# Kernel tuning notes

Measured on AMD Instinct MI355X. Metric: run time of the kernel, lower is better.

## Reference

```python
import jax, jax.numpy as jnp
import numpy as np

DIM = 1024
H = 16
D = DIM // H  # head_dim = 64
SCALE = 1.0 / np.sqrt(D)


def setup_inputs() -> dict:
    key = jax.random.key(0)
    ks = jax.random.split(key, 4)
    B, S = 4, 4096
    std = 1.0 / np.sqrt(DIM)
    return {
        "x": jax.random.normal(ks[0], (B, S, DIM), jnp.float32),
        "Wqkv": jax.random.normal(ks[1], (DIM, 3 * DIM), jnp.float32) * std,
        "bqkv": jnp.zeros((3 * DIM,), jnp.float32),
        "Wq": jax.random.normal(ks[2], (DIM, DIM), jnp.float32) * std,
        "bq": jnp.zeros((DIM,), jnp.float32),
        "Wproj": jax.random.normal(ks[3], (DIM, DIM), jnp.float32) * std,
        "bproj": jnp.zeros((DIM,), jnp.float32),
        "num_anchor_tokens": 512,
    }


def reference(x, Wqkv, bqkv, Wq, bq, Wproj, bproj, num_anchor_tokens):
    B, S, _ = x.shape
    A = num_anchor_tokens  # static Python int
    anchors = x[:, :A, :]          # (B, A, DIM)
    queries = x[:, A:, :]          # (B, Q, DIM)
    Q = S - A

    # Anchor tokens: full qkv projection
    qkv = anchors @ Wqkv + bqkv                      # (B, A, 3*DIM)
    qkv = qkv.reshape(B, A, 3, H, D)
    aq = jnp.transpose(qkv[:, :, 0], (0, 2, 1, 3))   # (B, H, A, D)
    ak = jnp.transpose(qkv[:, :, 1], (0, 2, 1, 3))   # (B, H, A, D)
    av = jnp.transpose(qkv[:, :, 2], (0, 2, 1, 3))   # (B, H, A, D)

    # Query tokens: query-only projection
    qq = (queries @ Wq + bq).reshape(B, Q, H, D)
    qq = jnp.transpose(qq, (0, 2, 1, 3))             # (B, H, Q, D)

    q_all = jnp.concatenate([aq, qq], axis=2)        # (B, H, S, D)

    # Everyone attends only to anchor keys/values
    scores = jnp.einsum("bhsd,bhad->bhsa", q_all, ak) * SCALE  # (B, H, S, A)
    attn = jax.nn.softmax(scores, axis=-1)
    out = jnp.einsum("bhsa,bhad->bhsd", attn, av)    # (B, H, S, D)
    out = jnp.transpose(out, (0, 2, 1, 3)).reshape(B, S, DIM)
    return out @ Wproj + bproj
```

## Files before the change

### kernel.cpp

```cpp
#include <hip/hip_runtime.h>
#include <hip/hip_bf16.h>

#define DIMC 1024
#define HC   16
#define DC   64
#define BC   4
#define SC   4096
#define ANC  512
#define QNC  3584
#define GK   1024
#define QSCALE (0.125f * 1.44269504088896f)

typedef __attribute__((ext_vector_type(4))) float f32x4;
typedef __attribute__((ext_vector_type(8))) short s16x8;
typedef __attribute__((ext_vector_type(4))) short s16x4;

__device__ inline short f2bf(float f) {
    unsigned u = __builtin_bit_cast(unsigned, f);
    u += 0x7fff + ((u >> 16) & 1);
    return (short)(u >> 16);
}
__device__ inline unsigned cvtpk(float lo, float hi) {
    unsigned d;
    asm("v_cvt_pk_bf16_f32 %0, %1, %2" : "=v"(d) : "v"(lo), "v"(hi));
    return d;
}

#define GLOAD16(gp, lp) __builtin_amdgcn_global_load_lds( \
    (const __attribute__((address_space(1))) void*)(gp),  \
    (__attribute__((address_space(3))) void*)(lp), 16, 0, 0)

__device__ __forceinline__ void tc_tile(
    const float* __restrict__ W, short* __restrict__ Wt, int K, int N,
    int bx, int by, float (*t)[33])
{
    const int tx = threadIdx.x & 31, ty = threadIdx.x >> 5;
    const int nt = bx * 32, kt = by * 32;
    #pragma unroll
    for (int j = 0; j < 4; ++j)
        t[ty + 8 * j][tx] = W[(size_t)(kt + ty + 8 * j) * N + nt + tx];
    __syncthreads();
    #pragma unroll
    for (int j = 0; j < 4; ++j)
        Wt[(size_t)(nt + ty + 8 * j) * K + kt + tx] = f2bf(t[tx][ty + 8 * j]);
}

__global__ __launch_bounds__(256) void prepass(
    const float* __restrict__ x, short* __restrict__ xb,
    const float* __restrict__ Wqkv, short* __restrict__ Wqkvt,
    const float* __restrict__ Wq, short* __restrict__ Wqt,
    const float* __restrict__ Wproj, short* __restrict__ Wprojt)
{
    __shared__ float t[32][33];
    const int b = blockIdx.x;
    if (b < 2048) {
        int i = b * 256 + threadIdx.x;
        for (; i < 4194304; i += 2048 * 256) {
            float4 v = ((const float4*)x)[i];
            s16x4 o = { f2bf(v.x), f2bf(v.y), f2bf(v.z), f2bf(v.w) };
            ((s16x4*)xb)[i] = o;
        }
    } else if (b < 5120) {
        const int z = b - 2048;
        tc_tile(Wqkv, Wqkvt, 1024, 3072, z % 96, z / 96, t);
    } else {
        const int z = b - 5120;
        const float* W = (z < 1024) ? Wq : Wproj;
        short* Wt = (z < 1024) ? Wqt : Wprojt;
        const int zz = z & 1023;
        tc_tile(W, Wt, 1024, 1024, zz & 31, zz >> 5, t);
    }
}

__device__ __forceinline__ void gemm_body(
    char* AB,
    const char* Arow0, const char* Brow0, const float* bias,
    float* outF, short* outQ, short* outK, short* outVt,
    int bm, int bn, int bb, int blocal, int rowOff, int mode)
{
    const int tid = threadIdx.x;
    const int wave = tid >> 6, lane = tid & 63;
    const int q = lane & 15, g = lane >> 4;
    const int wm = wave >> 1, wn = wave & 1;

    int srcOff[2], dstOff[2];
    #pragma unroll
    for (int p = 0; p < 2; ++p) {
        const int ca = p * 256 + tid;
        const int row = ca >> 2;
        const int c = (ca & 3) ^ ((row >> 1) & 3);
        srcOff[p] = row * (GK * 2) + c * 16;
        dstOff[p] = ca * 16;
    }

    f32x4 acc[4][4];
    #pragma unroll
    for (int i = 0; i < 4; ++i)
        #pragma unroll
        for (int j = 0; j < 4; ++j) acc[i][j] = (f32x4){0.f, 0.f, 0.f, 0.f};

    const int rc = ((g ^ ((q >> 1) & 3)) << 4);

#define STAGE(bufi, kt) do {                                            \
        const int kb_ = (kt) * 64;       \
        char* ab_ = AB + (bufi) * 8192;                                 \
        char* bb_ = AB + 24576 + (bufi) * 8192;                         \
        GLOAD16(Arow0 + srcOff[0] + kb_, ab_ + dstOff[0]);              \
        GLOAD16(Arow0 + srcOff[1] + kb_, ab_ + dstOff[1]);              \
        GLOAD16(Brow0 + srcOff[0] + kb_, bb_ + dstOff[0]);              \
        GLOAD16(Brow0 + srcOff[1] + kb_, bb_ + dstOff[1]);              \
    } while (0)

#define COMPUTE(bufi) do {                                              \
        const char* ab_ = AB + (bufi) * 8192;                           \
        const char* bb_ = AB + 24576 + (bufi) * 8192;                   \
        s16x8 aF[4], bF[4];                                             \
        _Pragma("unroll")                                               \
        for (int mi = 0; mi < 4; ++mi)                                  \
            aF[mi] = *(const s16x8*)(ab_ + (wm * 64 + mi * 16 + q) * 64 + rc); \
        _Pragma("unroll")                                               \
        for (int ni = 0; ni < 4; ++ni)                                  \
            bF[ni] = *(const s16x8*)(bb_ + (wn * 64 + ni * 16 + q) * 64 + rc); \
        _Pragma("unroll")                                               \
        for (int mi = 0; mi < 4; ++mi)                                  \
            _Pragma("unroll")                                           \
            for (int ni = 0; ni < 4; ++ni)                              \
                acc[mi][ni] = __builtin_amdgcn_mfma_f32_16x16x32_bf16(  \
                    aF[mi], bF[ni], acc[mi][ni], 0, 0, 0);              \
    } while (0)

#define PHASE4(stb, cb, kt) do {                                        \
        asm volatile("s_waitcnt vmcnt(4)" ::: "memory");                \
        __builtin_amdgcn_s_barrier();                                   \
        STAGE(stb, kt);                                                 \
        COMPUTE(cb);                                                    \
    } while (0)

    STAGE(0, 0);
    STAGE(1, 1);

    #pragma unroll 1
    for (int t = 0; t < 30; t += 3) {
        PHASE4(2, 0, t + 2);
        PHASE4(0, 1, t + 3);
        PHASE4(1, 2, t + 4);
    }
    asm volatile("s_waitcnt vmcnt(4)" ::: "memory");
    __builtin_amdgcn_s_barrier();
    COMPUTE(0);
    asm volatile("s_waitcnt vmcnt(0)" ::: "memory");
    __builtin_amdgcn_s_barrier();
    COMPUTE(1);

#undef PHASE4
#undef STAGE
#undef COMPUTE

    #pragma unroll
    for (int ni = 0; ni < 4; ++ni) {
        const int col = bn + wn * 64 + ni * 16 + q;
        const float bv = bias[col];
        #pragma unroll
        for (int mi = 0; mi < 4; ++mi) {
            const int rl0 = blocal + wm * 64 + mi * 16 + 4 * g;
            if (mode == 2) {
                const int grow = bm + wm * 64 + mi * 16 + 4 * g;
                #pragma unroll
                for (int r = 0; r < 4; ++r)
                    outF[(size_t)(grow + r) * 1024 + col] = acc[mi][ni][r] + bv;
            } else if (mode == 1) {
                const int h = col >> 6, d = col & 63;
                const size_t base = ((size_t)(bb * HC + h)) * SC + rowOff + rl0;
                #pragma unroll
                for (int r = 0; r < 4; ++r)
                    outQ[(base + r) * DC + d] = f2bf((acc[mi][ni][r] + bv) * QSCALE);
            } else {
                const int which = col >> 10;
                const int hd = col & 1023;
                const int h = hd >> 6, d = hd & 63;
                const size_t bh = (size_t)(bb * HC + h);
                if (which == 0) {
                    #pragma unroll
                    for (int r = 0; r < 4; ++r)
                        outQ[(bh * SC + rl0 + r) * DC + d] =
                            f2bf((acc[mi][ni][r] + bv) * QSCALE);
                } else if (which == 1) {
                    #pragma unroll
                    for (int r = 0; r < 4; ++r)
                        outK[(bh * ANC + rl0 + r) * DC + d] = f2bf(acc[mi][ni][r] + bv);
                } else {
                    union { s16x4 v; unsigned long long d8; } pk;
                    #pragma unroll
                    for (int r = 0; r < 4; ++r) pk.v[r] = f2bf(acc[mi][ni][r] + bv);
                    *(unsigned long long*)(outVt + (bh * DC + d) * ANC + rl0) = pk.d8;
                }
            }
        }
    }
}

__global__ __launch_bounds__(256) void gemm_k1k2(
    const short* __restrict__ xb,
    const short* __restrict__ Wqkvt, const float* __restrict__ bqkv,
    const short* __restrict__ Wqt,   const float* __restrict__ bq,
    short* __restrict__ Qb, short* __restrict__ Kb, short* __restrict__ Vtb)
{
    __shared__ __align__(16) char AB[49152];

    const int i = blockIdx.x;
    const char* Arow0; const char* Brow0; const float* bias;
    int bm, bn, bb, blocal, rowOff, mode;
    if (i < 384) {
        const int c = i & 7, j = i >> 3;
        bn = (j % 24) * 128;
        bm = ((j / 24) * 8 + c) * 128;
        bb = bm / ANC; blocal = bm % ANC; rowOff = 0; mode = 0;
        Arow0 = (const char*)(xb + ((size_t)bb * SC + blocal) * GK);
        Brow0 = (const char*)(Wqkvt + (size_t)bn * GK);
        bias = bqkv;
    } else {
        const int i2 = i - 384;
        const int c = i2 & 7, j = i2 >> 3;
        bn = (j % 8) * 128;
        bm = ((j / 8) * 8 + c) * 128;
        bb = bm / QNC; blocal = bm % QNC; rowOff = ANC; mode = 1;
        Arow0 = (const char*)(xb + ((size_t)bb * SC + ANC + blocal) * GK);
        Brow0 = (const char*)(Wqt + (size_t)bn * GK);
        bias = bq;
    }
    gemm_body(AB, Arow0, Brow0, bias,
              nullptr, Qb, Kb, Vtb, bm, bn, bb, blocal, rowOff, mode);
}

__global__ __launch_bounds__(256) void gemm_proj(
    const short* __restrict__ Abase, const short* __restrict__ Bt,
    const float* __restrict__ bias, float* __restrict__ outF)
{
    __shared__ __align__(16) char AB[49152];

    const int i = blockIdx.x;
    const int c = i & 7, j = i >> 3;
    const int bn = (j % 8) * 128;
    const int bm = ((j / 8) * 8 + c) * 128;
    const char* Arow0 = (const char*)(Abase + (size_t)bm * GK);
    const char* Brow0 = (const char*)(Bt + (size_t)bn * GK);
    gemm_body(AB, Arow0, Brow0, bias,
              outF, nullptr, nullptr, nullptr, bm, bn, 0, bm, 0, 2);
}

__global__ __launch_bounds__(512, 2) void attn_mfma(
    const short* __restrict__ Qb,
    const short* __restrict__ Kb,
    const short* __restrict__ Vtb,
    short* __restrict__ Aout)
{
    __shared__ __align__(16) char lds[147456];

    const int tid = threadIdx.x;
    const int wave = tid >> 6, lane = tid & 63;
    const int q = lane & 15, g = lane >> 4;
    const int q7 = q & 7;
    const int G = g ^ q7;
    const int bh = blockIdx.x >> 2;
    const int qc = blockIdx.x & 3;
    const int sbase = qc * 1024 + wave * 128;

    {
        const char* src = (const char*)(Kb + (size_t)bh * ANC * DC);
        #pragma unroll
        for (int l = 0; l < 8; ++l) {
            int i = l * 512 + tid;
            int row = i >> 3, cg = i & 7;
            union { float4 v; unsigned long long d[2]; } u;
            u.v = *(const float4*)(src + (size_t)i * 16);
            int kk = cg >> 2;
            int u0 = (2 * cg) & 7;
            int pc0 = 4 * kk + (u0 & 3);
            int hh = (u0 >> 2) << 3;
            int r7 = row & 7;
            char* dst = lds + row * 128;
            *(unsigned long long*)(dst + ((pc0 ^ r7) << 4) + hh) = u.d[0];
            *(unsigned long long*)(dst + (((pc0 + 1) ^ r7) << 4) + hh) = u.d[1];
        }
    }
    {
        const char* src = (const char*)(Vtb + (size_t)bh * DC * ANC);
        #pragma unroll
        for (int l = 0; l < 8; ++l) {
            int i = l * 512 + tid;
            int row = i >> 6, cg = i & 63;
            union { float4 v; unsigned long long d[2]; } u;
            u.v = *(const float4*)(src + (size_t)i * 16);
            int t2 = cg >> 2;
            int u0 = (2 * cg) & 7;
            int pc0 = 4 * t2 + (u0 & 3);
            int hh = (u0 >> 2) << 3;
            int r7 = row & 7;
            char* dst = lds + 65536 + row * 1024;
            *(unsigned long long*)(dst + ((pc0 ^ r7) << 4) + hh) = u.d[0];
            *(unsigned long long*)(dst + (((pc0 + 1) ^ r7) << 4) + hh) = u.d[1];
        }
    }
    __syncthreads();

    char* slot = lds + 131072 + wave * 2048;
    const int srow = lane >> 2, sc2 = lane & 3;
    const int sr7 = srow & 7;

    const int cgA = 2 * sc2, kkA = cgA >> 2, u0A = (2 * cgA) & 7;
    const int pcA = 4 * kkA + (u0A & 3), hA = (u0A >> 2) << 3;
    const int cgB = cgA + 1, kkB = cgB >> 2, u0B = (2 * cgB) & 7;
    const int pcB = 4 * kkB + (u0B & 3), hB = (u0B >> 2) << 3;
    const int wA0 = srow * 128 + ((pcA ^ sr7) << 4) + hA;
    const int wA1 = srow * 128 + (((pcA + 1) ^ sr7) << 4) + hA;
    const int wB0 = srow * 128 + ((pcB ^ sr7) << 4) + hB;
    const int wB1 = srow * 128 + (((pcB + 1) ^ sr7) << 4) + hB;
    const int wb0 = srow * 128 + (((sc2 * 2 + 0) ^ sr7) << 4);
    const int wb1 = srow * 128 + (((sc2 * 2 + 1) ^ sr7) << 4);
    const int sw = q7 << 4;

    const int off0 = G << 4, off1 = off0 ^ 64;
    const char* kb0 = lds + q * 128 + off0;
    const char* kb1 = lds + q * 128 + off1;
    const char* vregion = lds + 65536;
    const unsigned vo0 = (unsigned)((q +  0) * 1024 + off0);
    const unsigned vo1 = (unsigned)((q + 16) * 1024 + off0);
    const unsigned vo2 = (unsigned)((q + 32) * 1024 + off0);
    const unsigned vo3 = (unsigned)((q + 48) * 1024 + off0);

    const size_t qrow0 = (size_t)bh * SC;

    union { float4 v; unsigned long long d[2]; } gqA0, gqA1, gqB0, gqB1;
    {
        const char* QA = (const char*)(Qb + (qrow0 + sbase) * DC);
        gqA0.v = *(const float4*)(QA + lane * 32);
        gqA1.v = *(const float4*)(QA + lane * 32 + 16);
        const char* QB = QA + 16 * DC * 2;
        gqB0.v = *(const float4*)(QB + lane * 32);
        gqB1.v = *(const float4*)(QB + lane * 32 + 16);
    }

    for (int tp = 0; tp < 4; ++tp) {
        const int s0A = sbase + tp * 32;
        const int s0B = s0A + 16;

        *(unsigned long long*)(slot + wA0) = gqA0.d[0];
        *(unsigned long long*)(slot + wA1) = gqA0.d[1];
        *(unsigned long long*)(slot + wB0) = gqA1.d[0];
        *(unsigned long long*)(slot + wB1) = gqA1.d[1];
        __asm__ __volatile__("" ::: "memory");
        s16x8 qfA0 = *(const s16x8*)(slot + q * 128 + off0);
        s16x8 qfA1 = *(const s16x8*)(slot + q * 128 + off1);
        __asm__ __volatile__("" ::: "memory");
        *(unsigned long long*)(slot + wA0) = gqB0.d[0];
        *(unsigned long long*)(slot + wA1) = gqB0.d[1];
        *(unsigned long long*)(slot + wB0) = gqB1.d[0];
        *(unsigned long long*)(slot + wB1) = gqB1.d[1];
        __asm__ __volatile__("" ::: "memory");
        s16x8 qfB0 = *(const s16x8*)(slot + q * 128 + off0);
        s16x8 qfB1 = *(const s16x8*)(slot + q * 128 + off1);

        s16x8 pfA[16], pfB[16];
        float psA0 = 0.f, psA1 = 0.f, psA2 = 0.f, psA3 = 0.f;
        float psB0 = 0.f, psB1 = 0.f, psB2 = 0.f, psB3 = 0.f;
        __builtin_amdgcn_s_setprio(1);
        #pragma unroll
        for (int t2 = 0; t2 < 16; ++t2) {
            const int be = (2 * t2) * 2048, bo = be + 2048;
            s16x8 kfe0 = *(const s16x8*)(kb0 + be);
            s16x8 kfe1 = *(const s16x8*)(kb1 + be);
            f32x4 sA = (f32x4){0.f, 0.f, 0.f, 0.f};
            sA = __builtin_amdgcn_mfma_f32_16x16x32_bf16(kfe0, qfA0, sA, 0, 0, 0);
            sA = __builtin_amdgcn_mfma_f32_16x16x32_bf16(kfe1, qfA1, sA, 0, 0, 0);
            f32x4 sB = (f32x4){0.f, 0.f, 0.f, 0.f};
            sB = __builtin_amdgcn_mfma_f32_16x16x32_bf16(kfe0, qfB0, sB, 0, 0, 0);
            sB = __builtin_amdgcn_mfma_f32_16x16x32_bf16(kfe1, qfB1, sB, 0, 0, 0);
            s16x8 kfo0 = *(const s16x8*)(kb0 + bo);
            s16x8 kfo1 = *(const s16x8*)(kb1 + bo);
            f32x4 tA = (f32x4){0.f, 0.f, 0.f, 0.f};
            tA = __builtin_amdgcn_mfma_f32_16x16x32_bf16(kfo0, qfA0, tA, 0, 0, 0);
            tA = __builtin_amdgcn_mfma_f32_16x16x32_bf16(kfo1, qfA1, tA, 0, 0, 0);
            f32x4 tB = (f32x4){0.f, 0.f, 0.f, 0.f};
            tB = __builtin_amdgcn_mfma_f32_16x16x32_bf16(kfo0, qfB0, tB, 0, 0, 0);
            tB = __builtin_amdgcn_mfma_f32_16x16x32_bf16(kfo1, qfB1, tB, 0, 0, 0);

            float eA0 = exp2f(sA[0]), eA1 = exp2f(sA[1]);
            float eA2 = exp2f(sA[2]), eA3 = exp2f(sA[3]);
            float fA0 = exp2f(tA[0]), fA1 = exp2f(tA[1]);
            float fA2 = exp2f(tA[2]), fA3 = exp2f(tA[3]);
            psA0 += eA0 + fA0; psA1 += eA1 + fA1;
            psA2 += eA2 + fA2; psA3 += eA3 + fA3;
            float eB0 = exp2f(sB[0]), eB1 = exp2f(sB[1]);
            float eB2 = exp2f(sB[2]), eB3 = exp2f(sB[3]);
            float fB0 = exp2f(tB[0]), fB1 = exp2f(tB[1]);
            float fB2 = exp2f(tB[2]), fB3 = exp2f(tB[3]);
            psB0 += eB0 + fB0; psB1 += eB1 + fB1;
            psB2 += eB2 + fB2; psB3 += eB3 + fB3;

            union { s16x8 v; unsigned u[4]; } pkA, pkB;
            pkA.u[0] = cvtpk(eA0, eA1); pkA.u[1] = cvtpk(eA2, eA3);
            pkA.u[2] = cvtpk(fA0, fA1); pkA.u[3] = cvtpk(fA2, fA3);
            pfA[t2] = pkA.v;
            pkB.u[0] = cvtpk(eB0, eB1); pkB.u[1] = cvtpk(eB2, eB3);
            pkB.u[2] = cvtpk(fB0, fB1); pkB.u[3] = cvtpk(fB2, fB3);
            pfB[t2] = pkB.v;
        }
        __builtin_amdgcn_s_setprio(0);

        {
            const int snext = (tp < 3) ? (s0A + 32) : sbase;
            const char* QA = (const char*)(Qb + (qrow0 + snext) * DC);
            gqA0.v = *(const float4*)(QA + lane * 32);
            gqA1.v = *(const float4*)(QA + lane * 32 + 16);
            const char* QB = QA + 16 * DC * 2;
            gqB0.v = *(const float4*)(QB + lane * 32);
            gqB1.v = *(const float4*)(QB + lane * 32 + 16);
            __asm__ __volatile__("" :
                "+v"(gqA0.v.x), "+v"(gqA0.v.y), "+v"(gqA0.v.z), "+v"(gqA0.v.w),
                "+v"(gqA1.v.x), "+v"(gqA1.v.y), "+v"(gqA1.v.z), "+v"(gqA1.v.w),
                "+v"(gqB0.v.x), "+v"(gqB0.v.y), "+v"(gqB0.v.z), "+v"(gqB0.v.w),
                "+v"(gqB1.v.x), "+v"(gqB1.v.y), "+v"(gqB1.v.z), "+v"(gqB1.v.w));
        }

        float sumA = (psA0 + psA1) + (psA2 + psA3);
        sumA += __shfl_xor(sumA, 16);
        sumA += __shfl_xor(sumA, 32);
        const float rinvA = 1.0f / sumA;
        float sumB = (psB0 + psB1) + (psB2 + psB3);
        sumB += __shfl_xor(sumB, 16);
        sumB += __shfl_xor(sumB, 32);
        const float rinvB = 1.0f / sumB;

        f32x4 oaccA[4], oaccB[4];
        #pragma unroll
        for (int md = 0; md < 4; ++md) {
            oaccA[md] = (f32x4){0.f, 0.f, 0.f, 0.f};
            oaccB[md] = (f32x4){0.f, 0.f, 0.f, 0.f};
        }
        __builtin_amdgcn_s_setprio(1);
        #pragma unroll
        for (int t2 = 0; t2 < 16; ++t2) {
            const unsigned tx = (unsigned)(t2 << 6);
            s16x8 vf0 = *(const s16x8*)(vregion + (vo0 ^ tx));
            oaccA[0] = __builtin_amdgcn_mfma_f32_16x16x32_bf16(vf0, pfA[t2], oaccA[0], 0, 0, 0);
            oaccB[0] = __builtin_amdgcn_mfma_f32_16x16x32_bf16(vf0, pfB[t2], oaccB[0], 0, 0, 0);
            s16x8 vf1 = *(const s16x8*)(vregion + (vo1 ^ tx));
            oaccA[1] = __builtin_amdgcn_mfma_f32_16x16x32_bf16(vf1, pfA[t2], oaccA[1], 0, 0, 0);
            oaccB[1] = __builtin_amdgcn_mfma_f32_16x16x32_bf16(vf1, pfB[t2], oaccB[1], 0, 0, 0);
            s16x8 vf2 = *(const s16x8*)(vregion + (vo2 ^ tx));
            oaccA[2] = __builtin_amdgcn_mfma_f32_16x16x32_bf16(vf2, pfA[t2], oaccA[2], 0, 0, 0);
            oaccB[2] = __builtin_amdgcn_mfma_f32_16x16x32_bf16(vf2, pfB[t2], oaccB[2], 0, 0, 0);
            s16x8 vf3 = *(const s16x8*)(vregion + (vo3 ^ tx));
            oaccA[3] = __builtin_amdgcn_mfma_f32_16x16x32_bf16(vf3, pfA[t2], oaccA[3], 0, 0, 0);
            oaccB[3] = __builtin_amdgcn_mfma_f32_16x16x32_bf16(vf3, pfB[t2], oaccB[3], 0, 0, 0);
        }
        __builtin_amdgcn_s_setprio(0);

        __asm__ __volatile__("" ::: "memory");
        #pragma unroll
        for (int md = 0; md < 4; ++md) {
            union { unsigned long long d; unsigned u[2]; } ow;
            ow.u[0] = cvtpk(oaccA[md][0] * rinvA, oaccA[md][1] * rinvA);
            ow.u[1] = cvtpk(oaccA[md][2] * rinvA, oaccA[md][3] * rinvA);
            *(unsigned long long*)(slot + q * 128 + ((32 * md + 8 * g) ^ sw)) = ow.d;
        }
        __asm__ __volatile__("" ::: "memory");
        {
            float4 o0 = *(const float4*)(slot + wb0);
            float4 o1 = *(const float4*)(slot + wb1);
            char* Op = (char*)Aout +
                (((size_t)(bh >> 4) * SC + s0A + srow) * DIMC + (bh & 15) * DC) * 2 +
                sc2 * 32;
            *(float4*)(Op) = o0;
            *(float4*)(Op + 16) = o1;
        }
        __asm__ __volatile__("" ::: "memory");
        #pragma unroll
        for (int md = 0; md < 4; ++md) {
            union { unsigned long long d; unsigned u[2]; } ow;
            ow.u[0] = cvtpk(oaccB[md][0] * rinvB, oaccB[md][1] * rinvB);
            ow.u[1] = cvtpk(oaccB[md][2] * rinvB, oaccB[md][3] * rinvB);
            *(unsigned long long*)(slot + q * 128 + ((32 * md + 8 * g) ^ sw)) = ow.d;
        }
        __asm__ __volatile__("" ::: "memory");
        {
            float4 o0 = *(const float4*)(slot + wb0);
            float4 o1 = *(const float4*)(slot + wb1);
            char* Op = (char*)Aout +
                (((size_t)(bh >> 4) * SC + s0B + srow) * DIMC + (bh & 15) * DC) * 2 +
                sc2 * 32;
            *(float4*)(Op) = o0;
            *(float4*)(Op + 16) = o1;
        }
    }
}

extern "C" void kernel_launch(void* const* d_in, const int* in_sizes, int n_in,
                              void* d_out, int out_size, void* d_ws, size_t ws_size,
                              hipStream_t stream)
{
    (void)in_sizes; (void)n_in; (void)out_size; (void)ws_size;

    const float* x     = (const float*)d_in[0];
    const float* Wqkv  = (const float*)d_in[1];
    const float* bqkv  = (const float*)d_in[2];
    const float* Wq    = (const float*)d_in[3];
    const float* bq    = (const float*)d_in[4];
    const float* Wproj = (const float*)d_in[5];
    const float* bproj = (const float*)d_in[6];

    short* xb = (short*)d_out;
    short* Qb = xb + (size_t)16777216;
    short* Kb     = (short*)d_ws;
    short* Vtb    = Kb  + (size_t)2097152;
    short* Ab     = Vtb + (size_t)2097152;
    short* Wqkvt  = Ab  + (size_t)16777216;
    short* Wqt    = Wqkvt + (size_t)3145728;
    short* Wprojt = Wqt   + (size_t)1048576;

    prepass<<<dim3(7168), dim3(256), 0, stream>>>(
        x, xb, Wqkv, Wqkvt, Wq, Wqt, Wproj, Wprojt);

    gemm_k1k2<<<dim3(1280), dim3(256), 0, stream>>>(
        xb, Wqkvt, bqkv, Wqt, bq, Qb, Kb, Vtb);

    attn_mfma<<<dim3(256), dim3(512), 0, stream>>>(Qb, Kb, Vtb, Ab);

    gemm_proj<<<dim3(1024), dim3(256), 0, stream>>>(Ab, Wprojt, bproj, (float*)d_out);
}
```

Before: 173.1 us.

## Fuse fp32-to-bf16 conversion of x into QKV GEMM A-tile loading

New measurement: 172.0 us. No clear change (-0.6%).

```diff
diff --git a/kernel.cpp b/kernel.cpp
--- a/kernel.cpp
+++ b/kernel.cpp
@@ -46,25 +46,16 @@
 }
 
 __global__ __launch_bounds__(256) void prepass(
-    const float* __restrict__ x, short* __restrict__ xb,
     const float* __restrict__ Wqkv, short* __restrict__ Wqkvt,
     const float* __restrict__ Wq, short* __restrict__ Wqt,
     const float* __restrict__ Wproj, short* __restrict__ Wprojt)
 {
     __shared__ float t[32][33];
     const int b = blockIdx.x;
-    if (b < 2048) {
-        int i = b * 256 + threadIdx.x;
-        for (; i < 4194304; i += 2048 * 256) {
-            float4 v = ((const float4*)x)[i];
-            s16x4 o = { f2bf(v.x), f2bf(v.y), f2bf(v.z), f2bf(v.w) };
-            ((s16x4*)xb)[i] = o;
-        }
-    } else if (b < 5120) {
-        const int z = b - 2048;
-        tc_tile(Wqkv, Wqkvt, 1024, 3072, z % 96, z / 96, t);
+    if (b < 3072) {
+        tc_tile(Wqkv, Wqkvt, 1024, 3072, b % 96, b / 96, t);
     } else {
-        const int z = b - 5120;
+        const int z = b - 3072;
         const float* W = (z < 1024) ? Wq : Wproj;
         short* Wt = (z < 1024) ? Wqt : Wprojt;
         const int zz = z & 1023;
@@ -72,43 +63,88 @@
     }
 }
 
-__device__ __forceinline__ void gemm_body(
-    char* AB,
-    const char* Arow0, const char* Brow0, const float* bias,
-    float* outF, short* outQ, short* outK, short* outVt,
-    int bm, int bn, int bb, int blocal, int rowOff, int mode)
+__global__ __launch_bounds__(256, 3) void gemm_k1k2(
+    const float* __restrict__ x,
+    const short* __restrict__ Wqkvt, const float* __restrict__ bqkv,
+    const short* __restrict__ Wqt,   const float* __restrict__ bq,
+    short* __restrict__ Qb, short* __restrict__ Kb, short* __restrict__ Vtb)
 {
+    __shared__ __align__(16) char AB[49152];
+
     const int tid = threadIdx.x;
     const int wave = tid >> 6, lane = tid & 63;
     const int q = lane & 15, g = lane >> 4;
     const int wm = wave >> 1, wn = wave & 1;
 
-    int srcOff[2], dstOff[2];
+    const int i = blockIdx.x;
+    const char* ArowF; const char* Brow0; const float* bias;
+    int bb, blocal, rowOff, bn, mode;
+    if (i < 384) {
+        const int c = i & 7, j = i >> 3;
+        bn = (j % 24) * 128;
+        const int bm = ((j / 24) * 8 + c) * 128;
+        bb = bm / ANC; blocal = bm % ANC; rowOff = 0; mode = 0;
+        ArowF = (const char*)(x + ((size_t)bb * SC + blocal) * DIMC);
+        Brow0 = (const char*)(Wqkvt + (size_t)bn * GK);
+        bias = bqkv;
+    } else {
+        const int i2 = i - 384;
+        const int c = i2 & 7, j = i2 >> 3;
+        bn = (j % 8) * 128;
+        const int bm = ((j / 8) * 8 + c) * 128;
+        bb = bm / QNC; blocal = bm % QNC; rowOff = ANC; mode = 1;
+        ArowF = (const char*)(x + ((size_t)bb * SC + ANC + blocal) * DIMC);
+        Brow0 = (const char*)(Wqt + (size_t)bn * GK);
+        bias = bq;
+    }
+
+    int srcF[2], srcB[2], dstOff[2];
     #pragma unroll
     for (int p = 0; p < 2; ++p) {
         const int ca = p * 256 + tid;
         const int row = ca >> 2;
         const int c = (ca & 3) ^ ((row >> 1) & 3);
-        srcOff[p] = row * (GK * 2) + c * 16;
+        srcF[p] = row * 4096 + c * 32;
+        srcB[p] = row * (GK * 2) + c * 16;
         dstOff[p] = ca * 16;
     }
 
     f32x4 acc[4][4];
     #pragma unroll
-    for (int i = 0; i < 4; ++i)
-        #pragma unroll
-        for (int j = 0; j < 4; ++j) acc[i][j] = (f32x4){0.f, 0.f, 0.f, 0.f};
+    for (int a = 0; a < 4; ++a)
+        #pragma unroll
+        for (int b2 = 0; b2 < 4; ++b2) acc[a][b2] = (f32x4){0.f, 0.f, 0.f, 0.f};
 
     const int rc = ((g ^ ((q >> 1) & 3)) << 4);
 
-#define STAGE(bufi, kt) do {                                            \
-        const int kb_ = (kt) * 64;       \
+    float4 rA[3][4];
+
+#define ISSB(bufi, kt) do {                                             \
+        char* bb_ = AB + 24576 + (bufi) * 8192;                         \
+        GLOAD16(Brow0 + srcB[0] + (kt) * 64, bb_ + dstOff[0]);          \
+        GLOAD16(Brow0 + srcB[1] + (kt) * 64, bb_ + dstOff[1]);          \
+    } while (0)
+
+#define ISSA(s, kt) do {                                                \
+        rA[s][0] = *(const float4*)(ArowF + srcF[0] + (kt) * 128);      \
+        rA[s][1] = *(const float4*)(ArowF + srcF[0] + (kt) * 128 + 16); \
+        rA[s][2] = *(const float4*)(ArowF + srcF[1] + (kt) * 128);      \
+        rA[s][3] = *(const float4*)(ArowF + srcF[1] + (kt) * 128 + 16); \
+    } while (0)
+
+#define WRA(bufi, s) do {                                               \
         char* ab_ = AB + (bufi) * 8192;                                 \
-        char* bb_ = AB + 24576 + (bufi) * 8192;                         \
-        GLOAD16(Arow0 + srcOff[0] + kb_, ab_ + dstOff[0]);              \
-        GLOAD16(Arow0 + srcOff[1] + kb_, ab_ + dstOff[1]);              \
-        GLOAD16(Brow0 + srcOff[0] + kb_, bb_ + dstOff[0]);              \
-        GLOAD16(Brow0 + srcOff[1] + kb_, bb_ + dstOff[1]);              \
+        union { s16x8 v; unsigned u[4]; } w0, w1;                       \
+        w0.u[0] = cvtpk(rA[s][0].x, rA[s][0].y);                        \
+        w0.u[1] = cvtpk(rA[s][0].z, rA[s][0].w);                        \
+        w0.u[2] = cvtpk(rA[s][1].x, rA[s][1].y);                        \
+        w0.u[3] = cvtpk(rA[s][1].z, rA[s][1].w);                        \
+        w1.u[0] = cvtpk(rA[s][2].x, rA[s][2].y);                        \
+        w1.u[1] = cvtpk(rA[s][2].z, rA[s][2].w);                        \
+        w1.u[2] = cvtpk(rA[s][3].x, rA[s][3].y);                        \
+        w1.u[3] = cvtpk(rA[s][3].z, rA[s][3].w);                        \
+        *(s16x8*)(ab_ + dstOff[0]) = w0.v;                              \
+        *(s16x8*)(ab_ + dstOff[1]) = w1.v;                              \
     } while (0)
 
 #define COMPUTE(bufi) do {                                              \
@@ -129,32 +165,48 @@
                     aF[mi], bF[ni], acc[mi][ni], 0, 0, 0);              \
     } while (0)
 
-#define PHASE4(stb, cb, kt) do {                                        \
-        asm volatile("s_waitcnt vmcnt(4)" ::: "memory");                \
+#define PHF(cb, Bb, Wb, Ws, As, ktB, ktA) do {                          \
+        asm volatile("s_waitcnt vmcnt(6)" ::: "memory");                \
         __builtin_amdgcn_s_barrier();                                   \
-        STAGE(stb, kt);                                                 \
+        ISSB(Bb, ktB);                                                  \
+        ISSA(As, ktA);                                                  \
+        WRA(Wb, Ws);                                                    \
         COMPUTE(cb);                                                    \
     } while (0)
 
-    STAGE(0, 0);
-    STAGE(1, 1);
+    ISSA(0, 0);
+    ISSB(0, 0); ISSA(1, 1);
+    ISSB(1, 1); ISSA(2, 2);
+    asm volatile("s_waitcnt vmcnt(0)" ::: "memory");
+    WRA(0, 0);
+    asm volatile("s_waitcnt lgkmcnt(0)" ::: "memory");
 
     #pragma unroll 1
-    for (int t = 0; t < 30; t += 3) {
-        PHASE4(2, 0, t + 2);
-        PHASE4(0, 1, t + 3);
-        PHASE4(1, 2, t + 4);
-    }
-    asm volatile("s_waitcnt vmcnt(4)" ::: "memory");
+    for (int t = 0; t < 27; t += 3) {
+        PHF(0, 2, 1, 1, 0, t + 2, t + 3);
+        PHF(1, 0, 2, 2, 1, t + 3, t + 4);
+        PHF(2, 1, 0, 0, 2, t + 4, t + 5);
+    }
+    PHF(0, 2, 1, 1, 0, 29, 30);
+    PHF(1, 0, 2, 2, 1, 30, 31);
+    asm volatile("s_waitcnt vmcnt(6)" ::: "memory");
     __builtin_amdgcn_s_barrier();
+    ISSB(1, 31);
+    WRA(0, 0);
+    COMPUTE(2);
+    asm volatile("s_waitcnt vmcnt(2)" ::: "memory");
+    __builtin_amdgcn_s_barrier();
+    WRA(1, 1);
     COMPUTE(0);
     asm volatile("s_waitcnt vmcnt(0)" ::: "memory");
     __builtin_amdgcn_s_barrier();
     COMPUTE(1);
 
-#undef PHASE4
-#undef STAGE
+#undef PHF
 #undef COMPUTE
+#undef WRA
+#undef ISSA
+#undef ISSB
 
     #pragma unroll
     for (int ni = 0; ni < 4; ++ni) {
@@ -163,17 +215,16 @@
         #pragma unroll
         for (int mi = 0; mi < 4; ++mi) {
             const int rl0 = blocal + wm * 64 + mi * 16 + 4 * g;
-            if (mode == 2) {
-                const int grow = bm + wm * 64 + mi * 16 + 4 * g;
-                #pragma unroll
-                for (int r = 0; r < 4; ++r)
-                    outF[(size_t)(grow + r) * 1024 + col] = acc[mi][ni][r] + bv;
-            } else if (mode == 1) {
+            if (mode == 1) {
                 const int h = col >> 6, d = col & 63;
                 const size_t base = ((size_t)(bb * HC + h)) * SC + rowOff + rl0;
                 #pragma unroll
                 for (int r = 0; r < 4; ++r)
-                    outQ[(base + r) * DC + d] = f2bf((acc[mi][ni][r] + bv) * QSCALE);
+                    outQ_idx: ;
+                #pragma unroll
+                for (int r = 0; r < 4; ++r)
+                    Qb[(base + r) * DC + (col & 63)] =
+                        f2bf((acc[mi][ni][r] + bv) * QSCALE);
             } else {
                 const int which = col >> 10;
                 const int hd = col & 1023;
@@ -182,54 +233,21 @@
                 if (which == 0) {
                     #pragma unroll
                     for (int r = 0; r < 4; ++r)
-                        outQ[(bh * SC + rl0 + r) * DC + d] =
+                        Qb[(bh * SC + rl0 + r) * DC + d] =
                             f2bf((acc[mi][ni][r] + bv) * QSCALE);
                 } else if (which == 1) {
                     #pragma unroll
                     for (int r = 0; r < 4; ++r)
-                        outK[(bh * ANC + rl0 + r) * DC + d] = f2bf(acc[mi][ni][r] + bv);
+                        Kb[(bh * ANC + rl0 + r) * DC + d] = f2bf(acc[mi][ni][r] + bv);
                 } else {
                     union { s16x4 v; unsigned long long d8; } pk;
                     #pragma unroll
                     for (int r = 0; r < 4; ++r) pk.v[r] = f2bf(acc[mi][ni][r] + bv);
-                    *(unsigned long long*)(outVt + (bh * DC + d) * ANC + rl0) = pk.d8;
+                    *(unsigned long long*)(Vtb + (bh * DC + d) * ANC + rl0) = pk.d8;
                 }
             }
         }
     }
-}
-
-__global__ __launch_bounds__(256) void gemm_k1k2(
-    const short* __restrict__ xb,
-    const short* __restrict__ Wqkvt, const float* __restrict__ bqkv,
-    const short* __restrict__ Wqt,   const float* __restrict__ bq,
-    short* __restrict__ Qb, short* __restrict__ Kb, short* __restrict__ Vtb)
-{
-    __shared__ __align__(16) char AB[49152];
-
-    const int i = blockIdx.x;
-    const char* Arow0; const char* Brow0; const float* bias;
-    int bm, bn, bb, blocal, rowOff, mode;
-    if (i < 384) {
-        const int c = i & 7, j = i >> 3;
-        bn = (j % 24) * 128;
-        bm = ((j / 24) * 8 + c) * 128;
-        bb = bm / ANC; blocal = bm % ANC; rowOff = 0; mode = 0;
-        Arow0 = (const char*)(xb + ((size_t)bb * SC + blocal) * GK);
-        Brow0 = (const char*)(Wqkvt + (size_t)bn * GK);
-        bias = bqkv;
-    } else {
-        const int i2 = i - 384;
-        const int c = i2 & 7, j = i2 >> 3;
-        bn = (j % 8) * 128;
-        bm = ((j / 8) * 8 + c) * 128;
-        bb = bm / QNC; blocal = bm % QNC; rowOff = ANC; mode = 1;
-        Arow0 = (const char*)(xb + ((size_t)bb * SC + ANC + blocal) * GK);
-        Brow0 = (const char*)(Wqt + (size_t)bn * GK);
-        bias = bq;
-    }
-    gemm_body(AB, Arow0, Brow0, bias,
-              nullptr, Qb, Kb, Vtb, bm, bn, bb, blocal, rowOff, mode);
 }
 
 __global__ __launch_bounds__(256) void gemm_proj(
@@ -238,21 +256,106 @@
 {
     __shared__ __align__(16) char AB[49152];
 
+    const int tid = threadIdx.x;
+    const int wave = tid >> 6, lane = tid & 63;
+    const int q = lane & 15, g = lane >> 4;
+    const int wm = wave >> 1, wn = wave & 1;
+
     const int i = blockIdx.x;
-    const int c = i & 7, j = i >> 3;
+    const int c0 = i & 7, j = i >> 3;
     const int bn = (j % 8) * 128;
-    const int bm = ((j / 8) * 8 + c) * 128;
+    const int bm = ((j / 8) * 8 + c0) * 128;
     const char* Arow0 = (const char*)(Abase + (size_t)bm * GK);
     const char* Brow0 = (const char*)(Bt + (size_t)bn * GK);
-    gemm_body(AB, Arow0, Brow0, bias,
-              outF, nullptr, nullptr, nullptr, bm, bn, 0, bm, 0, 2);
+
+    int srcOff[2], dstOff[2];
+    #pragma unroll
+    for (int p = 0; p < 2; ++p) {
+        const int ca = p * 256 + tid;
+        const int row = ca >> 2;
+        const int c = (ca & 3) ^ ((row >> 1) & 3);
+        srcOff[p] = row * (GK * 2) + c * 16;
+        dstOff[p] = ca * 16;
+    }
+
+    f32x4 acc[4][4];
+    #pragma unroll
+    for (int a = 0; a < 4; ++a)
+        #pragma unroll
+        for (int b2 = 0; b2 < 4; ++b2) acc[a][b2] = (f32x4){0.f, 0.f, 0.f, 0.f};
+
+    const int rc = ((g ^ ((q >> 1) & 3)) << 4);
+
+#define STAGE(bufi, kt) do {                                            \
+        const int kb_ = (kt) * 64;                                      \
+        char* ab_ = AB + (bufi) * 8192;                                 \
+        char* bb_ = AB + 24576 + (bufi) * 8192;                         \
+        GLOAD16(Arow0 + srcOff[0] + kb_, ab_ + dstOff[0]);              \
+        GLOAD16(Arow0 + srcOff[1] + kb_, ab_ + dstOff[1]);              \
+        GLOAD16(Brow0 + srcOff[0] + kb_, bb_ + dstOff[0]);              \
+        GLOAD16(Brow0 + srcOff[1] + kb_, bb_ + dstOff[1]);              \
+    } while (0)
+
+#define COMPUTE(bufi) do {                                              \
+        const char* ab_ = AB + (bufi) * 8192;                           \
+        const char* bb_ = AB + 24576 + (bufi) * 8192;                   \
+        s16x8 aF[4], bF[4];                                             \
+        _Pragma("unroll")                                               \
+        for (int mi = 0; mi < 4; ++mi)                                  \
+            aF[mi] = *(const s16x8*)(ab_ + (wm * 64 + mi * 16 + q) * 64 + rc); \
+        _Pragma("unroll")                                               \
+        for (int ni = 0; ni < 4; ++ni)                                  \
+            bF[ni] = *(const s16x8*)(bb_ + (wn * 64 + ni * 16 + q) * 64 + rc); \
+        _Pragma("unroll")                                               \
+        for (int mi = 0; mi < 4; ++mi)                                  \
+            _Pragma("unroll")                                           \
+            for (int ni = 0; ni < 4; ++ni)                              \
+                acc[mi][ni] = __builtin_amdgcn_mfma_f32_16x16x32_bf16(  \
+                    aF[mi], bF[ni], acc[mi][ni], 0, 0, 0);              \
+    } while (0)
+
+#define PHASE4(stb, cb, kt) do {                                        \
+        asm volatile("s_waitcnt vmcnt(4)" ::: "memory");                \
+        __builtin_amdgcn_s_barrier();                                   \
+        STAGE(stb, kt);                                                 \
+        COMPUTE(cb);                                                    \
+    } while (0)
+
+    STAGE(0, 0);
+    STAGE(1, 1);
+    #pragma unroll 1
+    for (int t = 0; t < 30; t += 3) {
+        PHASE4(2, 0, t + 2);
+        PHASE4(0, 1, t + 3);
+        PHASE4(1, 2, t + 4);
+    }
+    asm volatile("s_waitcnt vmcnt(4)" ::: "memory");
+    __builtin_amdgcn_s_barrier();
+    COMPUTE(0);
+    asm volatile("s_waitcnt vmcnt(0)" ::: "memory");
+    __builtin_amdgcn_s_barrier();
+    COMPUTE(1);
+#undef PHASE4
+#undef STAGE
+#undef COMPUTE
+
+    #pragma unroll
+    for (int ni = 0; ni < 4; ++ni) {
+        const int col = bn + wn * 64 + ni * 16 + q;
+        const float bv = bias[col];
+        #pragma unroll
+        for (int mi = 0; mi < 4; ++mi) {
+            const int grow = bm + wm * 64 + mi * 16 + 4 * g;
+            #pragma unroll
+            for (int r = 0; r < 4; ++r)
+                outF[(size_t)(grow + r) * 1024 + col] = acc[mi][ni][r] + bv;
+        }
+    }
 }
 
 __global__ __launch_bounds__(512, 2) void attn_mfma(
-    const short* __restrict__ Qb,
-    const short* __restrict__ Kb,
-    const short* __restrict__ Vtb,
-    short* __restrict__ Aout)
+    const short* __restrict__ Qb, const short* __restrict__ Kb,
+    const short* __restrict__ Vtb, short* __restrict__ Aout)
 {
     __shared__ __align__(16) char lds[147456];
 
@@ -509,8 +612,7 @@
     const float* Wproj = (const float*)d_in[5];
     const float* bproj = (const float*)d_in[6];
 
-    short* xb = (short*)d_out;
-    short* Qb = xb + (size_t)16777216;
+    short* Qb = (short*)d_out + (size_t)16777216;
     short* Kb     = (short*)d_ws;
     short* Vtb    = Kb  + (size_t)2097152;
     short* Ab     = Vtb + (size_t)2097152;
@@ -518,11 +620,11 @@
     short* Wqt    = Wqkvt + (size_t)3145728;
     short* Wprojt = Wqt   + (size_t)1048576;
 
-    prepass<<<dim3(7168), dim3(256), 0, stream>>>(
-        x, xb, Wqkv, Wqkvt, Wq, Wqt, Wproj, Wprojt);
+    prepass<<<dim3(5120), dim3(256), 0, stream>>>(
+        Wqkv, Wqkvt, Wq, Wqt, Wproj, Wprojt);
 
     gemm_k1k2<<<dim3(1280), dim3(256), 0, stream>>>(
-        xb, Wqkvt, bqkv, Wqt, bq, Qb, Kb, Vtb);
+        x, Wqkvt, bqkv, Wqt, bq, Qb, Kb, Vtb);
 
     attn_mfma<<<dim3(256), dim3(512), 0, stream>>>(Qb, Kb, Vtb, Ab);
 
```
